# Performance work log

Hardware: AMD Instinct MI355X
Metric: run time of the kernel (lower is better)

Reference implementation:

```python
import jax, jax.numpy as jnp
import numpy as np

N_NODES = 50000
N_EDGES = 800000
IN_DIM = 128
OUT_DIM = 64
NEG_SLOPE = 0.01  # torch F.leaky_relu default


def setup_inputs() -> dict:
    key = jax.random.key(0)
    k1, k2, k3, k4, k5 = jax.random.split(key, 5)
    h = jax.random.normal(k1, (N_NODES, IN_DIM), dtype=jnp.float32)
    src = jax.random.randint(k2, (N_EDGES,), 0, N_NODES, dtype=jnp.int32)
    dst = jnp.sort(jax.random.randint(k3, (N_EDGES,), 0, N_NODES, dtype=jnp.int32))
    fc_w = jax.random.normal(k4, (OUT_DIM, IN_DIM), dtype=jnp.float32) * (1.0 / np.sqrt(IN_DIM))
    attn_w = jax.random.normal(k5, (1, 2 * OUT_DIM), dtype=jnp.float32) * (1.0 / np.sqrt(2 * OUT_DIM))
    return {"h": h, "src": src, "dst": dst, "fc_w": fc_w, "attn_w": attn_w}


def reference(h, src, dst, fc_w, attn_w):
    # z = fc(h)                                   [N, D_out]
    z = h @ fc_w.T
    # edge attention: leaky_relu(attn_fc([z_src || z_dst]))  -> split attn weight
    a_src = attn_w[0, :OUT_DIM]   # [D_out]
    a_dst = attn_w[0, OUT_DIM:]   # [D_out]
    z_src = z[src]                # [E, D_out] gather
    e = jax.nn.leaky_relu(z_src @ a_src + z[dst] @ a_dst, negative_slope=NEG_SLOPE)  # [E]
    # segment softmax over incoming edges of each dst node
    e_max = jax.ops.segment_max(e, dst, num_segments=N_NODES)       # [N]
    e_exp = jnp.exp(e - e_max[dst])                                 # [E]
    e_sum = jax.ops.segment_sum(e_exp, dst, num_segments=N_NODES)   # [N]
    alpha = e_exp / e_sum[dst]                                      # [E]
    # weighted scatter-sum aggregation
    h_out = jax.ops.segment_sum(alpha[:, None] * z_src, dst, num_segments=N_NODES)  # [N, D_out]
    return h_out
```

## Files before the change

### kernel.cpp

```cpp
#include <hip/hip_runtime.h>
#include <hip/hip_bf16.h>
#include <math.h>

#define N_NODES 50000
#define N_EDGES 800000
#define IN_DIM 128
#define OUT_DIM 64
#define NEG_SLOPE 0.01f
#define TILE_E 512

typedef unsigned short u16;
typedef unsigned int   u32;
typedef __attribute__((ext_vector_type(8))) short bf16x8_t;
typedef __attribute__((ext_vector_type(4))) float f32x4_t;

static __device__ __forceinline__ u16 f2bf(float x) {
    __hip_bfloat16 b = __float2bfloat16(x);
    return __builtin_bit_cast(u16, b);
}
static __device__ __forceinline__ float bflo(u32 w) { return __uint_as_float(w << 16); }
static __device__ __forceinline__ float bfhi(u32 w) { return __uint_as_float(w & 0xffff0000u); }

__global__ __launch_bounds__(256) void gemm_fused_kernel(
    const float* __restrict__ h, const float* __restrict__ fc_w,
    const float* __restrict__ attn_w, const int* __restrict__ dst,
    u16* __restrict__ zb, float* __restrict__ s_src, float* __restrict__ s_dst,
    int* __restrict__ row_ptr)
{
    __shared__ u16 wlds[OUT_DIM][IN_DIM + 8];

    const int tid  = threadIdx.x;
    const int lane = tid & 63;
    const int wid  = blockIdx.x * 4 + (tid >> 6);
    const int row  = lane & 15;
    const int kq   = lane >> 4;

    for (int idx = tid; idx < OUT_DIM * IN_DIM / 2; idx += 256) {
        const int d  = idx >> 6;
        const int kk = idx & 63;
        const float2 f = ((const float2*)fc_w)[idx];
        const u32 w = ((u32)f2bf(f.y) << 16) | (u32)f2bf(f.x);
        *(u32*)&wlds[d][2 * kk] = w;
    }
    __syncthreads();

    if (wid < N_NODES / 16) {
        const int n0 = wid * 16;

        bf16x8_t afr[4];
        const float* hrow = h + (size_t)(n0 + row) * IN_DIM + 8 * kq;
#pragma unroll
        for (int kc = 0; kc < 4; ++kc) {
            const float4 f0 = *(const float4*)(hrow + 32 * kc);
            const float4 f1 = *(const float4*)(hrow + 32 * kc + 4);
            bf16x8_t a;
            a[0] = (short)f2bf(f0.x); a[1] = (short)f2bf(f0.y);
            a[2] = (short)f2bf(f0.z); a[3] = (short)f2bf(f0.w);
            a[4] = (short)f2bf(f1.x); a[5] = (short)f2bf(f1.y);
            a[6] = (short)f2bf(f1.z); a[7] = (short)f2bf(f1.w);
            afr[kc] = a;
        }

        f32x4_t acc[4];
#pragma unroll
        for (int dt = 0; dt < 4; ++dt) {
            f32x4_t c = {0.f, 0.f, 0.f, 0.f};
#pragma unroll
            for (int kc = 0; kc < 4; ++kc) {
                const bf16x8_t bfr =
                    *(const bf16x8_t*)&wlds[dt * 16 + row][32 * kc + 8 * kq];
                c = __builtin_amdgcn_mfma_f32_16x16x32_bf16(afr[kc], bfr, c, 0, 0, 0);
            }
            acc[dt] = c;
        }

#pragma unroll
        for (int dt = 0; dt < 4; ++dt)
#pragma unroll
            for (int r = 0; r < 4; ++r)
                zb[(size_t)(n0 + 4 * kq + r) * OUT_DIM + dt * 16 + row] = f2bf(acc[dt][r]);

        float a_s[4], a_d[4];
#pragma unroll
        for (int dt = 0; dt < 4; ++dt) {
            a_s[dt] = attn_w[dt * 16 + row];
            a_d[dt] = attn_w[OUT_DIM + dt * 16 + row];
        }
#pragma unroll
        for (int r = 0; r < 4; ++r) {
            float ps = 0.f, pd = 0.f;
#pragma unroll
            for (int dt = 0; dt < 4; ++dt) {
                ps = fmaf(acc[dt][r], a_s[dt], ps);
                pd = fmaf(acc[dt][r], a_d[dt], pd);
            }
#pragma unroll
            for (int mm = 1; mm < 16; mm <<= 1) {
                ps += __shfl_xor(ps, mm);
                pd += __shfl_xor(pd, mm);
            }
            if (row == 0) {
                const int n = n0 + 4 * kq + r;
                s_src[n] = ps;
                s_dst[n] = pd;
            }
        }
    }

    const int gt = blockIdx.x * 256 + tid;
    if (gt <= N_NODES) {
        int lo = 0, hi = N_EDGES;
        while (lo < hi) {
            const int mid = (lo + hi) >> 1;
            if (dst[mid] < gt) lo = mid + 1; else hi = mid;
        }
        row_ptr[gt] = lo;
    }
}

__global__ __launch_bounds__(256) void aggregate_kernel(
    const int* __restrict__ src, const int* __restrict__ dst,
    const int* __restrict__ row_ptr,
    const u16* __restrict__ zb, const float* __restrict__ s_src,
    const float* __restrict__ s_dst, float* __restrict__ out)
{
    __shared__ uint2 ep[TILE_E];

    const int tid = threadIdx.x;
    const int g   = tid >> 4;
    const int sub = tid & 15;
    const int nb  = blockIdx.x * 16;
    const int n   = nb + g;

    const int E0 = row_ptr[nb];
    const int E1 = row_ptr[nb + 16];
    const int e0 = row_ptr[n];
    const int e1 = row_ptr[n + 1];

    float denom = 0.f;
    float acc0 = 0.f, acc1 = 0.f, acc2 = 0.f, acc3 = 0.f;

    for (int t0 = E0; t0 < E1; t0 += TILE_E) {
        const int tend = (t0 + TILE_E < E1) ? (t0 + TILE_E) : E1;

        for (int idx = t0 + tid; idx < tend; idx += 256) {
            const int se = src[idx];
            const int de = dst[idx];
            float t = s_src[se] + s_dst[de];
            t = (t > 0.f) ? t : t * NEG_SLOPE;
            ep[idx - t0] = make_uint2((u32)se, __float_as_uint(__expf(t)));
        }
        __syncthreads();

        const int l0 = ((e0 > t0) ? e0 : t0) - t0;
        const int l1 = ((e1 < tend) ? e1 : tend) - t0;
#pragma unroll 4
        for (int j = l0; j < l1; ++j) {
            const uint2 sp = ep[j];
            const float pj = __uint_as_float(sp.y);
            const uint2 w = *(const uint2*)(zb + (size_t)sp.x * OUT_DIM + 4 * sub);
            denom += pj;
            acc0 = fmaf(pj, bflo(w.x), acc0);
            acc1 = fmaf(pj, bfhi(w.x), acc1);
            acc2 = fmaf(pj, bflo(w.y), acc2);
            acc3 = fmaf(pj, bfhi(w.y), acc3);
        }
        __syncthreads();
    }

    const float inv = (denom > 0.f) ? (1.f / denom) : 0.f;
    *(float4*)(out + (size_t)n * OUT_DIM + 4 * sub) =
        make_float4(acc0 * inv, acc1 * inv, acc2 * inv, acc3 * inv);
}

extern "C" void kernel_launch(void* const* d_in, const int* in_sizes, int n_in,
                              void* d_out, int out_size, void* d_ws, size_t ws_size,
                              hipStream_t stream)
{
    const float* h      = (const float*)d_in[0];
    const int*   src    = (const int*)  d_in[1];
    const int*   dst    = (const int*)  d_in[2];
    const float* fc_w   = (const float*)d_in[3];
    const float* attn_w = (const float*)d_in[4];
    float*       out    = (float*)d_out;

    char* ws = (char*)d_ws;
    u16* zb = (u16*)ws;
    ws += ((size_t)N_NODES * OUT_DIM * sizeof(u16) + 255) & ~(size_t)255;
    float* s_src = (float*)ws;
    ws += ((size_t)N_NODES * sizeof(float) + 255) & ~(size_t)255;
    float* s_dst = (float*)ws;
    ws += ((size_t)N_NODES * sizeof(float) + 255) & ~(size_t)255;
    int* row_ptr = (int*)ws;
    (void)ws_size;

    const int gemm_blocks = (N_NODES / 16 + 3) / 4;
    gemm_fused_kernel<<<gemm_blocks, 256, 0, stream>>>(
        h, fc_w, attn_w, dst, zb, s_src, s_dst, row_ptr);
    aggregate_kernel<<<N_NODES / 16, 256, 0, stream>>>(
        src, dst, row_ptr, zb, s_src, s_dst, out);
}
```

Before: 38.28 us.

## Build row_ptr by scanning dst boundaries and widen aggregate to 32 nodes per block

row_ptr is now built by having each thread read four consecutive dst values and write the CSR offsets at segment boundaries, replacing one binary search per node. The aggregation kernel now handles 32 destination nodes per block with 8 lanes per node. Each lane loads 16 bytes of bf16 features and keeps 8 accumulators, and the edge tile grows to 768 so one tile usually covers a block's edges. The goal is fewer, wider gather loads and less search work, at the cost of fewer blocks and more serial work per lane.

```diff
diff --git a/kernel.cpp b/kernel.cpp
--- a/kernel.cpp
+++ b/kernel.cpp
@@ -7,7 +7,8 @@
 #define IN_DIM 128
 #define OUT_DIM 64
 #define NEG_SLOPE 0.01f
-#define TILE_E 512
+#define TILE_E 768
+#define AGG_NPB 32
 
 typedef unsigned short u16;
 typedef unsigned int   u32;
@@ -107,14 +108,20 @@
         }
     }
 
-    const int gt = blockIdx.x * 256 + tid;
-    if (gt <= N_NODES) {
-        int lo = 0, hi = N_EDGES;
-        while (lo < hi) {
-            const int mid = (lo + hi) >> 1;
-            if (dst[mid] < gt) lo = mid + 1; else hi = mid;
-        }
-        row_ptr[gt] = lo;
+    const int t = blockIdx.x * 256 + tid;
+    if (t < N_EDGES / 4) {
+        const int eb = 4 * t;
+        const int4 d4 = *(const int4*)(dst + eb);
+        int prev = (eb == 0) ? -1 : dst[eb - 1];
+        const int dd[4] = {d4.x, d4.y, d4.z, d4.w};
+#pragma unroll
+        for (int k = 0; k < 4; ++k) {
+            const int cur = dd[k];
+            for (int n = prev + 1; n <= cur; ++n) row_ptr[n] = eb + k;
+            prev = cur;
+        }
+        if (eb + 4 == N_EDGES)
+            for (int n = prev + 1; n <= N_NODES; ++n) row_ptr[n] = N_EDGES;
     }
 }
 
@@ -127,28 +134,32 @@
     __shared__ uint2 ep[TILE_E];
 
     const int tid = threadIdx.x;
-    const int g   = tid >> 4;
-    const int sub = tid & 15;
-    const int nb  = blockIdx.x * 16;
+    const int g   = tid >> 3;
+    const int sub = tid & 7;
+    const int nb  = blockIdx.x * AGG_NPB;
     const int n   = nb + g;
+    const int ntop = (nb + AGG_NPB < N_NODES) ? (nb + AGG_NPB) : N_NODES;
 
     const int E0 = row_ptr[nb];
-    const int E1 = row_ptr[nb + 16];
-    const int e0 = row_ptr[n];
-    const int e1 = row_ptr[n + 1];
+    const int E1 = row_ptr[ntop];
+    const bool act = n < N_NODES;
+    const int e0 = act ? row_ptr[n] : E1;
+    const int e1 = act ? row_ptr[n + 1] : E1;
 
     float denom = 0.f;
-    float acc0 = 0.f, acc1 = 0.f, acc2 = 0.f, acc3 = 0.f;
+    float a0 = 0.f, a1 = 0.f, a2 = 0.f, a3 = 0.f;
+    float a4 = 0.f, a5 = 0.f, a6 = 0.f, a7 = 0.f;
 
     for (int t0 = E0; t0 < E1; t0 += TILE_E) {
         const int tend = (t0 + TILE_E < E1) ? (t0 + TILE_E) : E1;
 
+        __syncthreads();
         for (int idx = t0 + tid; idx < tend; idx += 256) {
             const int se = src[idx];
             const int de = dst[idx];
-            float t = s_src[se] + s_dst[de];
-            t = (t > 0.f) ? t : t * NEG_SLOPE;
-            ep[idx - t0] = make_uint2((u32)se, __float_as_uint(__expf(t)));
+            float tt = s_src[se] + s_dst[de];
+            tt = (tt > 0.f) ? tt : tt * NEG_SLOPE;
+            ep[idx - t0] = make_uint2((u32)se, __float_as_uint(__expf(tt)));
         }
         __syncthreads();
 
@@ -158,19 +169,21 @@
         for (int j = l0; j < l1; ++j) {
             const uint2 sp = ep[j];
             const float pj = __uint_as_float(sp.y);
-            const uint2 w = *(const uint2*)(zb + (size_t)sp.x * OUT_DIM + 4 * sub);
+            const uint4 w = *(const uint4*)(zb + (size_t)sp.x * OUT_DIM + 8 * sub);
             denom += pj;
-            acc0 = fmaf(pj, bflo(w.x), acc0);
-            acc1 = fmaf(pj, bfhi(w.x), acc1);
-            acc2 = fmaf(pj, bflo(w.y), acc2);
-            acc3 = fmaf(pj, bfhi(w.y), acc3);
-        }
-        __syncthreads();
-    }
-
-    const float inv = (denom > 0.f) ? (1.f / denom) : 0.f;
-    *(float4*)(out + (size_t)n * OUT_DIM + 4 * sub) =
-        make_float4(acc0 * inv, acc1 * inv, acc2 * inv, acc3 * inv);
+            a0 = fmaf(pj, bflo(w.x), a0);  a1 = fmaf(pj, bfhi(w.x), a1);
+            a2 = fmaf(pj, bflo(w.y), a2);  a3 = fmaf(pj, bfhi(w.y), a3);
+            a4 = fmaf(pj, bflo(w.z), a4);  a5 = fmaf(pj, bfhi(w.z), a5);
+            a6 = fmaf(pj, bflo(w.w), a6);  a7 = fmaf(pj, bfhi(w.w), a7);
+        }
+    }
+
+    if (act) {
+        const float inv = (denom > 0.f) ? (1.f / denom) : 0.f;
+        float* op = out + (size_t)n * OUT_DIM + 8 * sub;
+        *(float4*)(op)     = make_float4(a0 * inv, a1 * inv, a2 * inv, a3 * inv);
+        *(float4*)(op + 4) = make_float4(a4 * inv, a5 * inv, a6 * inv, a7 * inv);
+    }
 }
 
 extern "C" void kernel_launch(void* const* d_in, const int* in_sizes, int n_in,
@@ -197,6 +210,7 @@
     const int gemm_blocks = (N_NODES / 16 + 3) / 4;
     gemm_fused_kernel<<<gemm_blocks, 256, 0, stream>>>(
         h, fc_w, attn_w, dst, zb, s_src, s_dst, row_ptr);
-    aggregate_kernel<<<N_NODES / 16, 256, 0, stream>>>(
+    const int agg_blocks = (N_NODES + AGG_NPB - 1) / AGG_NPB;
+    aggregate_kernel<<<agg_blocks, 256, 0, stream>>>(
         src, dst, row_ptr, zb, s_src, s_dst, out);
 }
```

After: 33.88 us, median of 2. 1.13x faster.
